# Optimization experiments

Hardware: AMD Instinct MI355X
Metric: run time of the kernel (lower is better)

## Reference

```python
import jax, jax.numpy as jnp
import numpy as np
import math

B, S, D, V = 16, 512, 64, 32000
MAX_SEQ = 512
TEMP = 1.0
EPS = 1e-12


def setup_inputs() -> dict:
    key = jax.random.key(0)
    k0, k1, k2, k3, k4 = jax.random.split(key, 5)
    tokens = jax.random.randint(k0, (B, S), 0, V)
    token_emb = jax.random.normal(k1, (V, D), dtype=jnp.float32) * 0.02
    lin_w1 = jax.random.normal(k2, (D, D), dtype=jnp.float32) * (1.0 / math.sqrt(D))
    lin_w2 = jax.random.normal(k3, (D, D), dtype=jnp.float32) * (1.0 / math.sqrt(D))
    edge_scale = jnp.full((1,), 0.1, dtype=jnp.float32)  # nn.Parameter init 0.1
    out_w = jax.random.normal(k4, (V, D), dtype=jnp.float32) * 0.02
    return {"tokens": tokens, "token_emb": token_emb, "lin_w1": lin_w1,
            "lin_w2": lin_w2, "edge_scale": edge_scale, "out_w": out_w}


def _embed(tokens, token_emb):
    # polar positional components (seq_len <= max_seq_len branch)
    pos = jnp.arange(S, dtype=jnp.float32)
    thetas = 2.0 * math.pi * (pos / MAX_SEQ)
    rs = 0.3 + 0.6 * (pos / (MAX_SEQ - 1))
    e0 = (rs * jnp.cos(thetas))[None, :, None]          # [1,S,1]
    e1 = (rs * jnp.sin(thetas))[None, :, None]          # [1,S,1]
    tok = token_emb[tokens][:, :, : D - 2]              # [B,S,D-2]
    emb = jnp.concatenate([jnp.broadcast_to(e0, (tok.shape[0], S, 1)),
                           jnp.broadcast_to(e1, (tok.shape[0], S, 1)),
                           tok], axis=-1)               # [B,S,D]
    norms = jnp.sqrt(jnp.clip(jnp.einsum('bsd,bsd->bs', emb, emb), EPS, None))
    return emb / norms[:, :, None]


def _attention(emb):
    # pairwise Euclidean distance attention, diagonal distance zeroed
    n2 = jnp.einsum('bsd,bsd->bs', emb, emb)                      # [B,S]
    dots = jnp.einsum('bqd,bkd->bqk', emb, emb)                   # [B,S,S]
    sq = n2[:, :, None] + n2[:, None, :] - 2.0 * dots
    dist = jnp.sqrt(jnp.clip(sq, EPS, None))
    dist = dist * (1.0 - jnp.eye(S, dtype=dist.dtype))[None]      # eye_mask
    return jax.nn.softmax(-dist / TEMP, axis=-1)                  # [B,S,S]


def reference(tokens, token_emb, lin_w1, lin_w2, edge_scale, out_w):
    emb = _embed(tokens, token_emb)            # [B,S,D]
    attn = _attention(emb)                     # [B,S,S]
    h = emb
    for w in (lin_w1, lin_w2):
        # message passing: x_j -> lin(x_j), edge weight = attn * edge_scale,
        # scatter-add over all incoming edges == batched attn @ h
        h = edge_scale[0] * jnp.einsum('bqk,bkd->bqd', attn, h @ w.T)
    logits = jnp.einsum('bsd,vd->bsv', h, out_w)   # [B,S,V]
    return logits
```

## Files before the change

kernel.cpp:

```cpp
#include <hip/hip_runtime.h>
#include <hip/hip_bf16.h>


#define S_ 512
#define D_ 64
#define V_ 32000

typedef __attribute__((ext_vector_type(8))) __bf16 bf16x8;
typedef __attribute__((ext_vector_type(4))) float f32x4;

__device__ inline unsigned short f2bf(float x) {
    __hip_bfloat16 h = __float2bfloat16(x);
    return __builtin_bit_cast(unsigned short, h);
}

__global__ __launch_bounds__(256) void embed_kernel(const int* __restrict__ tokens,
                                                    const float* __restrict__ temb,
                                                    float* __restrict__ emb,
                                                    float* __restrict__ n2) {
    int row  = blockIdx.x * 4 + (threadIdx.x >> 6);
    int lane = threadIdx.x & 63;
    int s    = row & (S_ - 1);
    int tok  = tokens[row];
    float val;
    if (lane < 2) {
        float fs    = (float)s;
        float theta = 6.283185307179586f * (fs * (1.0f / 512.0f));
        float r     = 0.3f + 0.6f * (fs * (1.0f / 511.0f));
        val = (lane == 0) ? r * cosf(theta) : r * sinf(theta);
    } else {
        val = temb[tok * D_ + lane - 2];
    }
    float ss = val * val;
#pragma unroll
    for (int off = 32; off; off >>= 1) ss += __shfl_xor(ss, off, 64);
    float nrm = sqrtf(fmaxf(ss, 1e-12f));
    float e   = val / nrm;
    emb[row * D_ + lane] = e;
    float nn = e * e;
#pragma unroll
    for (int off = 32; off; off >>= 1) nn += __shfl_xor(nn, off, 64);
    if (lane == 0) n2[row] = nn;
}

__global__ __launch_bounds__(128) void attn_kernel(const float* __restrict__ emb,
                                                   const float* __restrict__ n2,
                                                   const float* __restrict__ edge_scale,
                                                   float* __restrict__ attn_u,
                                                   float* __restrict__ invs) {
    __shared__ float qs[16][68];
    __shared__ float ks[64][68];
    __shared__ float n2qs[16];
    __shared__ float n2ks[64];
    int b  = blockIdx.x >> 5;
    int q0 = (blockIdx.x & 31) * 16;
    int t  = threadIdx.x;
    const float* ebase = emb + (size_t)b * S_ * D_;
#pragma unroll
    for (int j = 0; j < 2; ++j) {
        int f4 = t + j * 128;
        int r = f4 >> 4, c4 = (f4 & 15) * 4;
        *reinterpret_cast<float4*>(&qs[r][c4]) =
            *reinterpret_cast<const float4*>(&ebase[(q0 + r) * D_ + c4]);
    }
    if (t < 16) n2qs[t] = n2[b * S_ + q0 + t];

    int qg = t >> 4;
    int kg = t & 15;
    float rs[2] = {0.f, 0.f};

    for (int kt = 0; kt < 8; ++kt) {
        int k0 = kt * 64;
        __syncthreads();
#pragma unroll
        for (int j = 0; j < 8; ++j) {
            int f4 = t + j * 128;
            int r = f4 >> 4, c4 = (f4 & 15) * 4;
            *reinterpret_cast<float4*>(&ks[r][c4]) =
                *reinterpret_cast<const float4*>(&ebase[(k0 + r) * D_ + c4]);
        }
        if (t < 64) n2ks[t] = n2[b * S_ + k0 + t];
        __syncthreads();

        f32x4 acc[2][4];
#pragma unroll
        for (int i = 0; i < 2; ++i)
#pragma unroll
            for (int j = 0; j < 4; ++j) acc[i][j] = (f32x4){0.f, 0.f, 0.f, 0.f};
#pragma unroll
        for (int dc = 0; dc < 16; ++dc) {
            f32x4 qv[2], kv[4];
#pragma unroll
            for (int i = 0; i < 2; ++i) qv[i] = *reinterpret_cast<f32x4*>(&qs[qg * 2 + i][dc * 4]);
#pragma unroll
            for (int j = 0; j < 4; ++j) kv[j] = *reinterpret_cast<f32x4*>(&ks[kg * 4 + j][dc * 4]);
#pragma unroll
            for (int i = 0; i < 2; ++i)
#pragma unroll
                for (int j = 0; j < 4; ++j) acc[i][j] += qv[i] * kv[j];
        }
#pragma unroll
        for (int i = 0; i < 2; ++i) {
            int q = qg * 2 + i;
            float4 ev;
            float* evp = &ev.x;
#pragma unroll
            for (int j = 0; j < 4; ++j) {
                int k = kg * 4 + j;
                f32x4 a = acc[i][j];
                float dot = (a[0] + a[1]) + (a[2] + a[3]);
                float sq  = n2qs[q] + n2ks[k] - 2.0f * dot;
                evp[j] = (q0 + q == k0 + k) ? 1.0f : __expf(-sqrtf(fmaxf(sq, 1e-12f)));
            }
            rs[i] += (ev.x + ev.y) + (ev.z + ev.w);
            *reinterpret_cast<float4*>(
                &attn_u[((size_t)(b * S_ + q0 + q)) * S_ + k0 + kg * 4]) = ev;
        }
    }
    float scale = edge_scale[0];
#pragma unroll
    for (int i = 0; i < 2; ++i) {
#pragma unroll
        for (int off = 1; off < 16; off <<= 1) rs[i] += __shfl_xor(rs[i], off, 64);
        if (kg == 0) invs[b * S_ + q0 + qg * 2 + i] = scale / rs[i];
    }
}

__global__ __launch_bounds__(256) void proj_kernel(const float* __restrict__ h,
                                                   const float* __restrict__ w,
                                                   float* __restrict__ out) {
    __shared__ float ws[64][68];
    __shared__ float hs[16][68];
    int t  = threadIdx.x;
    int r0 = blockIdx.x * 16;
#pragma unroll
    for (int j = 0; j < 4; ++j) {
        int f4 = t + j * 256;
        int r = f4 >> 4, c4 = (f4 & 15) * 4;
        *reinterpret_cast<float4*>(&ws[r][c4]) =
            *reinterpret_cast<const float4*>(&w[r * D_ + c4]);
    }
    {
        int r = t >> 4, c4 = (t & 15) * 4;
        *reinterpret_cast<float4*>(&hs[r][c4]) =
            *reinterpret_cast<const float4*>(&h[(r0 + r) * D_ + c4]);
    }
    __syncthreads();
    int q = t >> 4, dh = t & 15;
    f32x4 acc[4];
#pragma unroll
    for (int dj = 0; dj < 4; ++dj) acc[dj] = (f32x4){0.f, 0.f, 0.f, 0.f};
#pragma unroll
    for (int ec = 0; ec < 16; ++ec) {
        f32x4 hv = *reinterpret_cast<f32x4*>(&hs[q][ec * 4]);
#pragma unroll
        for (int dj = 0; dj < 4; ++dj) {
            f32x4 wv = *reinterpret_cast<f32x4*>(&ws[dh * 4 + dj][ec * 4]);
            acc[dj] += hv * wv;
        }
    }
    float4 r;
    r.x = (acc[0][0] + acc[0][1]) + (acc[0][2] + acc[0][3]);
    r.y = (acc[1][0] + acc[1][1]) + (acc[1][2] + acc[1][3]);
    r.z = (acc[2][0] + acc[2][1]) + (acc[2][2] + acc[2][3]);
    r.w = (acc[3][0] + acc[3][1]) + (acc[3][2] + acc[3][3]);
    *reinterpret_cast<float4*>(&out[(r0 + q) * D_ + dh * 4]) = r;
}

template <bool BF16OUT>
__global__ __launch_bounds__(128) void prop_kernel(const float* __restrict__ attn_u,
                                                   const float* __restrict__ tmat,
                                                   const float* __restrict__ invs,
                                                   float* __restrict__ outf,
                                                   unsigned short* __restrict__ outb) {
    __shared__ float As[16][68];
    __shared__ float Ts[64][68];
    int b  = blockIdx.x >> 5;
    int q0 = (blockIdx.x & 31) * 16;
    int t  = threadIdx.x;
    int qg = t >> 4, dh = t & 15;
    f32x4 acc[2];
#pragma unroll
    for (int i = 0; i < 2; ++i) acc[i] = (f32x4){0.f, 0.f, 0.f, 0.f};
    const float* abase = attn_u + ((size_t)b * S_ + q0) * S_;
    const float* tbase = tmat + (size_t)b * S_ * D_;
    for (int kt = 0; kt < 8; ++kt) {
        int k0 = kt * 64;
        __syncthreads();
#pragma unroll
        for (int j = 0; j < 2; ++j) {
            int f4 = t + j * 128;
            int r = f4 >> 4, c4 = (f4 & 15) * 4;
            *reinterpret_cast<float4*>(&As[r][c4]) =
                *reinterpret_cast<const float4*>(&abase[(size_t)r * S_ + k0 + c4]);
        }
#pragma unroll
        for (int j = 0; j < 8; ++j) {
            int f4 = t + j * 128;
            int r = f4 >> 4, c4 = (f4 & 15) * 4;
            *reinterpret_cast<float4*>(&Ts[r][c4]) =
                *reinterpret_cast<const float4*>(&tbase[(k0 + r) * D_ + c4]);
        }
        __syncthreads();
#pragma unroll
        for (int kc = 0; kc < 16; ++kc) {
            f32x4 tv[4];
#pragma unroll
            for (int ks = 0; ks < 4; ++ks)
                tv[ks] = *reinterpret_cast<f32x4*>(&Ts[kc * 4 + ks][dh * 4]);
#pragma unroll
            for (int i = 0; i < 2; ++i) {
                f32x4 av = *reinterpret_cast<f32x4*>(&As[qg * 2 + i][kc * 4]);
#pragma unroll
                for (int ks = 0; ks < 4; ++ks) acc[i] += av[ks] * tv[ks];
            }
        }
    }
#pragma unroll
    for (int i = 0; i < 2; ++i) {
        int row = b * S_ + q0 + qg * 2 + i;
        float inv = invs[row];
        size_t rowbase = (size_t)row * D_ + dh * 4;
        if (BF16OUT) {
            ushort4 r;
            r.x = f2bf(inv * acc[i][0]); r.y = f2bf(inv * acc[i][1]);
            r.z = f2bf(inv * acc[i][2]); r.w = f2bf(inv * acc[i][3]);
            *reinterpret_cast<ushort4*>(&outb[rowbase]) = r;
        } else {
            *reinterpret_cast<float4*>(&outf[rowbase]) =
                make_float4(inv * acc[i][0], inv * acc[i][1],
                            inv * acc[i][2], inv * acc[i][3]);
        }
    }
}

__global__ __launch_bounds__(256) void cast_kernel(const float* __restrict__ in,
                                                   unsigned short* __restrict__ out, int n) {
    int i = (blockIdx.x * 256 + threadIdx.x) * 4;
    if (i >= n) return;
    float4 v = *reinterpret_cast<const float4*>(in + i);
    ushort4 r;
    r.x = f2bf(v.x); r.y = f2bf(v.y); r.z = f2bf(v.z); r.w = f2bf(v.w);
    *reinterpret_cast<ushort4*>(out + i) = r;
}

__global__ __launch_bounds__(256) void logits_kernel(const unsigned short* __restrict__ hb,
                                                     const unsigned short* __restrict__ wb,
                                                     float* __restrict__ out) {
    __shared__ float Ct[2][16][260];
    int bid = blockIdx.x;
    int nt = bid % 125, mt = bid / 125;
    int n0 = nt * 256, m0 = mt * 128;
    int wave = threadIdx.x >> 6, lane = threadIdx.x & 63;
    int lr = lane & 15, lh = lane >> 4;

    bf16x8 a[2][2][2];
#pragma unroll
    for (int c = 0; c < 2; ++c)
#pragma unroll
        for (int ns = 0; ns < 2; ++ns)
#pragma unroll
            for (int kh = 0; kh < 2; ++kh)
                a[c][ns][kh] = *reinterpret_cast<const bf16x8*>(
                    wb + (size_t)(n0 + wave * 64 + c * 32 + ns * 16 + lr) * D_ + kh * 32 + lh * 8);

    for (int ms = 0; ms < 8; ++ms) {
        const unsigned short* hrow = hb + (size_t)(m0 + ms * 16 + lr) * D_ + lh * 8;
        bf16x8 b0 = *reinterpret_cast<const bf16x8*>(hrow);
        bf16x8 b1 = *reinterpret_cast<const bf16x8*>(hrow + 32);
        f32x4 acc[2][2];
#pragma unroll
        for (int c = 0; c < 2; ++c)
#pragma unroll
            for (int ns = 0; ns < 2; ++ns) {
                acc[c][ns] = (f32x4){0.f, 0.f, 0.f, 0.f};
                acc[c][ns] = __builtin_amdgcn_mfma_f32_16x16x32_bf16(a[c][ns][0], b0, acc[c][ns], 0, 0, 0);
                acc[c][ns] = __builtin_amdgcn_mfma_f32_16x16x32_bf16(a[c][ns][1], b1, acc[c][ns], 0, 0, 0);
            }

        float* Lw = &Ct[ms & 1][lr][wave * 64];
#pragma unroll
        for (int c = 0; c < 2; ++c)
#pragma unroll
            for (int ns = 0; ns < 2; ++ns) {
                f32x4 v = acc[c][ns];
                *reinterpret_cast<float4*>(Lw + c * 32 + ns * 16 + lh * 4) =
                    make_float4(v[0], v[1], v[2], v[3]);
            }
        __syncthreads();

#pragma unroll
        for (int j = 0; j < 4; ++j) {
            int row = wave * 4 + j;
            const float* Lr = &Ct[ms & 1][row][lane * 4];
            float4 v = *reinterpret_cast<const float4*>(Lr);
            *reinterpret_cast<float4*>(out + (size_t)(m0 + ms * 16 + row) * V_ + n0 + lane * 4) = v;
        }
    }
}

extern "C" void kernel_launch(void* const* d_in, const int* in_sizes, int n_in,
                              void* d_out, int out_size, void* d_ws, size_t ws_size,
                              hipStream_t stream) {
    const int*   tokens = (const int*)d_in[0];
    const float* temb   = (const float*)d_in[1];
    const float* w1     = (const float*)d_in[2];
    const float* w2     = (const float*)d_in[3];
    const float* escale = (const float*)d_in[4];
    const float* outw   = (const float*)d_in[5];
    float*       out    = (float*)d_out;

    char* tail = (char*)d_out + 1048576000ull - 23068672ull;
    float* attn = (float*)(tail);
    float* emb  = (float*)(tail + 16777216);
    float* t1   = (float*)(tail + 18874368);
    float* h1   = (float*)(tail + 20971520);

    char* ws = (char*)d_ws;
    unsigned short* hb   = (unsigned short*)(ws);
    unsigned short* wb   = (unsigned short*)(ws + 1048576);
    float*          n2   = (float*)(ws + 5144576);
    float*          invs = (float*)(ws + 5177344);

    embed_kernel<<<2048, 256, 0, stream>>>(tokens, temb, emb, n2);
    attn_kernel<<<512, 128, 0, stream>>>(emb, n2, escale, attn, invs);
    cast_kernel<<<2000, 256, 0, stream>>>(outw, wb, V_ * D_);
    proj_kernel<<<512, 256, 0, stream>>>(emb, w1, t1);
    prop_kernel<false><<<512, 128, 0, stream>>>(attn, t1, invs, h1, nullptr);
    proj_kernel<<<512, 256, 0, stream>>>(h1, w2, t1);
    prop_kernel<true><<<512, 128, 0, stream>>>(attn, t1, invs, nullptr, hb);
    logits_kernel<<<8000, 256, 0, stream>>>(hb, wb, out);
}
```

Measured before the change: 290.9 us.

## Fold W2 into output weights and reassociate W1 after attention propagation

```diff
diff --git a/kernel.cpp b/kernel.cpp
--- a/kernel.cpp
+++ b/kernel.cpp
@@ -14,33 +14,77 @@
     return __builtin_bit_cast(unsigned short, h);
 }
 
-__global__ __launch_bounds__(256) void embed_kernel(const int* __restrict__ tokens,
-                                                    const float* __restrict__ temb,
-                                                    float* __restrict__ emb,
-                                                    float* __restrict__ n2) {
-    int row  = blockIdx.x * 4 + (threadIdx.x >> 6);
-    int lane = threadIdx.x & 63;
-    int s    = row & (S_ - 1);
-    int tok  = tokens[row];
-    float val;
-    if (lane < 2) {
-        float fs    = (float)s;
-        float theta = 6.283185307179586f * (fs * (1.0f / 512.0f));
-        float r     = 0.3f + 0.6f * (fs * (1.0f / 511.0f));
-        val = (lane == 0) ? r * cosf(theta) : r * sinf(theta);
+__global__ __launch_bounds__(256) void embed_wprime_kernel(const int* __restrict__ tokens,
+                                                           const float* __restrict__ temb,
+                                                           float* __restrict__ emb,
+                                                           float* __restrict__ n2,
+                                                           const float* __restrict__ outw,
+                                                           const float* __restrict__ w2,
+                                                           unsigned short* __restrict__ wb) {
+    __shared__ float os[16][68];
+    __shared__ float w2t[64][68];
+    int bid = blockIdx.x;
+    if (bid < 2048) {
+        int row  = bid * 4 + (threadIdx.x >> 6);
+        int lane = threadIdx.x & 63;
+        int s    = row & (S_ - 1);
+        int tok  = tokens[row];
+        float val;
+        if (lane < 2) {
+            float fs    = (float)s;
+            float theta = 6.283185307179586f * (fs * (1.0f / 512.0f));
+            float r     = 0.3f + 0.6f * (fs * (1.0f / 511.0f));
+            val = (lane == 0) ? r * cosf(theta) : r * sinf(theta);
+        } else {
+            val = temb[tok * D_ + lane - 2];
+        }
+        float ss = val * val;
+#pragma unroll
+        for (int off = 32; off; off >>= 1) ss += __shfl_xor(ss, off, 64);
+        float nrm = sqrtf(fmaxf(ss, 1e-12f));
+        float e   = val / nrm;
+        emb[row * D_ + lane] = e;
+        float nn = e * e;
+#pragma unroll
+        for (int off = 32; off; off >>= 1) nn += __shfl_xor(nn, off, 64);
+        if (lane == 0) n2[row] = nn;
     } else {
-        val = temb[tok * D_ + lane - 2];
-    }
-    float ss = val * val;
-#pragma unroll
-    for (int off = 32; off; off >>= 1) ss += __shfl_xor(ss, off, 64);
-    float nrm = sqrtf(fmaxf(ss, 1e-12f));
-    float e   = val / nrm;
-    emb[row * D_ + lane] = e;
-    float nn = e * e;
-#pragma unroll
-    for (int off = 32; off; off >>= 1) nn += __shfl_xor(nn, off, 64);
-    if (lane == 0) n2[row] = nn;
+        int r0 = (bid - 2048) * 16;
+        int t  = threadIdx.x;
+        {
+            int r = t >> 4, c4 = (t & 15) * 4;
+            *reinterpret_cast<float4*>(&os[r][c4]) =
+                *reinterpret_cast<const float4*>(&outw[(size_t)(r0 + r) * D_ + c4]);
+        }
+#pragma unroll
+        for (int j = 0; j < 4; ++j) {
+            int f4 = t + j * 256;
+            int d = f4 >> 4, c4 = (f4 & 15) * 4;
+            float4 v = *reinterpret_cast<const float4*>(&w2[d * D_ + c4]);
+            w2t[c4 + 0][d] = v.x; w2t[c4 + 1][d] = v.y;
+            w2t[c4 + 2][d] = v.z; w2t[c4 + 3][d] = v.w;
+        }
+        __syncthreads();
+        int q = t >> 4, eh = t & 15;
+        f32x4 acc[4];
+#pragma unroll
+        for (int ej = 0; ej < 4; ++ej) acc[ej] = (f32x4){0.f, 0.f, 0.f, 0.f};
+#pragma unroll
+        for (int dc = 0; dc < 16; ++dc) {
+            f32x4 ov = *reinterpret_cast<f32x4*>(&os[q][dc * 4]);
+#pragma unroll
+            for (int ej = 0; ej < 4; ++ej) {
+                f32x4 wv = *reinterpret_cast<f32x4*>(&w2t[eh * 4 + ej][dc * 4]);
+                acc[ej] += ov * wv;
+            }
+        }
+        ushort4 r;
+        r.x = f2bf((acc[0][0] + acc[0][1]) + (acc[0][2] + acc[0][3]));
+        r.y = f2bf((acc[1][0] + acc[1][1]) + (acc[1][2] + acc[1][3]));
+        r.z = f2bf((acc[2][0] + acc[2][1]) + (acc[2][2] + acc[2][3]));
+        r.w = f2bf((acc[3][0] + acc[3][1]) + (acc[3][2] + acc[3][3]));
+        *reinterpret_cast<ushort4*>(&wb[(size_t)(r0 + q) * D_ + eh * 4]) = r;
+    }
 }
 
 __global__ __launch_bounds__(128) void attn_kernel(const float* __restrict__ emb,
@@ -126,52 +170,104 @@
     }
 }
 
-__global__ __launch_bounds__(256) void proj_kernel(const float* __restrict__ h,
-                                                   const float* __restrict__ w,
-                                                   float* __restrict__ out) {
-    __shared__ float ws[64][68];
-    __shared__ float hs[16][68];
+__global__ __launch_bounds__(128) void prop_proj_kernel(const float* __restrict__ attn_u,
+                                                        const float* __restrict__ hsrc,
+                                                        const float* __restrict__ w1,
+                                                        const float* __restrict__ invs,
+                                                        float* __restrict__ outf) {
+    __shared__ float As[16][68];
+    __shared__ float Ts[64][68];
+    __shared__ float ws1[64][68];
+    __shared__ float gs[16][68];
+    int b  = blockIdx.x >> 5;
+    int q0 = (blockIdx.x & 31) * 16;
     int t  = threadIdx.x;
-    int r0 = blockIdx.x * 16;
-#pragma unroll
-    for (int j = 0; j < 4; ++j) {
-        int f4 = t + j * 256;
+    int qg = t >> 4, dh = t & 15;
+#pragma unroll
+    for (int j = 0; j < 8; ++j) {
+        int f4 = t + j * 128;
         int r = f4 >> 4, c4 = (f4 & 15) * 4;
-        *reinterpret_cast<float4*>(&ws[r][c4]) =
-            *reinterpret_cast<const float4*>(&w[r * D_ + c4]);
-    }
-    {
-        int r = t >> 4, c4 = (t & 15) * 4;
-        *reinterpret_cast<float4*>(&hs[r][c4]) =
-            *reinterpret_cast<const float4*>(&h[(r0 + r) * D_ + c4]);
+        *reinterpret_cast<float4*>(&ws1[r][c4]) =
+            *reinterpret_cast<const float4*>(&w1[r * D_ + c4]);
+    }
+    f32x4 acc[2];
+#pragma unroll
+    for (int i = 0; i < 2; ++i) acc[i] = (f32x4){0.f, 0.f, 0.f, 0.f};
+    const float* abase = attn_u + ((size_t)b * S_ + q0) * S_;
+    const float* tbase = hsrc + (size_t)b * S_ * D_;
+    for (int kt = 0; kt < 8; ++kt) {
+        int k0 = kt * 64;
+        __syncthreads();
+#pragma unroll
+        for (int j = 0; j < 2; ++j) {
+            int f4 = t + j * 128;
+            int r = f4 >> 4, c4 = (f4 & 15) * 4;
+            *reinterpret_cast<float4*>(&As[r][c4]) =
+                *reinterpret_cast<const float4*>(&abase[(size_t)r * S_ + k0 + c4]);
+        }
+#pragma unroll
+        for (int j = 0; j < 8; ++j) {
+            int f4 = t + j * 128;
+            int r = f4 >> 4, c4 = (f4 & 15) * 4;
+            *reinterpret_cast<float4*>(&Ts[r][c4]) =
+                *reinterpret_cast<const float4*>(&tbase[(k0 + r) * D_ + c4]);
+        }
+        __syncthreads();
+#pragma unroll
+        for (int kc = 0; kc < 16; ++kc) {
+            f32x4 tv[4];
+#pragma unroll
+            for (int ks = 0; ks < 4; ++ks)
+                tv[ks] = *reinterpret_cast<f32x4*>(&Ts[kc * 4 + ks][dh * 4]);
+#pragma unroll
+            for (int i = 0; i < 2; ++i) {
+                f32x4 av = *reinterpret_cast<f32x4*>(&As[qg * 2 + i][kc * 4]);
+#pragma unroll
+                for (int ks = 0; ks < 4; ++ks) acc[i] += av[ks] * tv[ks];
+            }
+        }
+    }
+#pragma unroll
+    for (int i = 0; i < 2; ++i) {
+        f32x4 v = acc[i];
+        *reinterpret_cast<float4*>(&gs[qg * 2 + i][dh * 4]) =
+            make_float4(v[0], v[1], v[2], v[3]);
     }
     __syncthreads();
-    int q = t >> 4, dh = t & 15;
-    f32x4 acc[4];
-#pragma unroll
-    for (int dj = 0; dj < 4; ++dj) acc[dj] = (f32x4){0.f, 0.f, 0.f, 0.f};
-#pragma unroll
-    for (int ec = 0; ec < 16; ++ec) {
-        f32x4 hv = *reinterpret_cast<f32x4*>(&hs[q][ec * 4]);
-#pragma unroll
-        for (int dj = 0; dj < 4; ++dj) {
-            f32x4 wv = *reinterpret_cast<f32x4*>(&ws[dh * 4 + dj][ec * 4]);
-            acc[dj] += hv * wv;
-        }
-    }
-    float4 r;
-    r.x = (acc[0][0] + acc[0][1]) + (acc[0][2] + acc[0][3]);
-    r.y = (acc[1][0] + acc[1][1]) + (acc[1][2] + acc[1][3]);
-    r.z = (acc[2][0] + acc[2][1]) + (acc[2][2] + acc[2][3]);
-    r.w = (acc[3][0] + acc[3][1]) + (acc[3][2] + acc[3][3]);
-    *reinterpret_cast<float4*>(&out[(r0 + q) * D_ + dh * 4]) = r;
-}
-
-template <bool BF16OUT>
+    f32x4 acc2[2][4];
+#pragma unroll
+    for (int i = 0; i < 2; ++i)
+#pragma unroll
+        for (int dj = 0; dj < 4; ++dj) acc2[i][dj] = (f32x4){0.f, 0.f, 0.f, 0.f};
+#pragma unroll
+    for (int dc = 0; dc < 16; ++dc) {
+        f32x4 wv[4];
+#pragma unroll
+        for (int dj = 0; dj < 4; ++dj)
+            wv[dj] = *reinterpret_cast<f32x4*>(&ws1[dh * 4 + dj][dc * 4]);
+#pragma unroll
+        for (int i = 0; i < 2; ++i) {
+            f32x4 gv = *reinterpret_cast<f32x4*>(&gs[qg * 2 + i][dc * 4]);
+#pragma unroll
+            for (int dj = 0; dj < 4; ++dj) acc2[i][dj] += gv * wv[dj];
+        }
+    }
+#pragma unroll
+    for (int i = 0; i < 2; ++i) {
+        int row = b * S_ + q0 + qg * 2 + i;
+        float inv = invs[row];
+        float4 r;
+        r.x = inv * ((acc2[i][0][0] + acc2[i][0][1]) + (acc2[i][0][2] + acc2[i][0][3]));
+        r.y = inv * ((acc2[i][1][0] + acc2[i][1][1]) + (acc2[i][1][2] + acc2[i][1][3]));
+        r.z = inv * ((acc2[i][2][0] + acc2[i][2][1]) + (acc2[i][2][2] + acc2[i][2][3]));
+        r.w = inv * ((acc2[i][3][0] + acc2[i][3][1]) + (acc2[i][3][2] + acc2[i][3][3]));
+        *reinterpret_cast<float4*>(&outf[(size_t)row * D_ + dh * 4]) = r;
+    }
+}
+
 __global__ __launch_bounds__(128) void prop_kernel(const float* __restrict__ attn_u,
                                                    const float* __restrict__ tmat,
                                                    const float* __restrict__ invs,
-                                                   float* __restrict__ outf,
                                                    unsigned short* __restrict__ outb) {
     __shared__ float As[16][68];
     __shared__ float Ts[64][68];
@@ -220,28 +316,11 @@
     for (int i = 0; i < 2; ++i) {
         int row = b * S_ + q0 + qg * 2 + i;
         float inv = invs[row];
-        size_t rowbase = (size_t)row * D_ + dh * 4;
-        if (BF16OUT) {
-            ushort4 r;
-            r.x = f2bf(inv * acc[i][0]); r.y = f2bf(inv * acc[i][1]);
-            r.z = f2bf(inv * acc[i][2]); r.w = f2bf(inv * acc[i][3]);
-            *reinterpret_cast<ushort4*>(&outb[rowbase]) = r;
-        } else {
-            *reinterpret_cast<float4*>(&outf[rowbase]) =
-                make_float4(inv * acc[i][0], inv * acc[i][1],
-                            inv * acc[i][2], inv * acc[i][3]);
-        }
-    }
-}
-
-__global__ __launch_bounds__(256) void cast_kernel(const float* __restrict__ in,
-                                                   unsigned short* __restrict__ out, int n) {
-    int i = (blockIdx.x * 256 + threadIdx.x) * 4;
-    if (i >= n) return;
-    float4 v = *reinterpret_cast<const float4*>(in + i);
-    ushort4 r;
-    r.x = f2bf(v.x); r.y = f2bf(v.y); r.z = f2bf(v.z); r.w = f2bf(v.w);
-    *reinterpret_cast<ushort4*>(out + i) = r;
+        ushort4 r;
+        r.x = f2bf(inv * acc[i][0]); r.y = f2bf(inv * acc[i][1]);
+        r.z = f2bf(inv * acc[i][2]); r.w = f2bf(inv * acc[i][3]);
+        *reinterpret_cast<ushort4*>(&outb[(size_t)row * D_ + dh * 4]) = r;
+    }
 }
 
 __global__ __launch_bounds__(256) void logits_kernel(const unsigned short* __restrict__ hb,
@@ -313,8 +392,7 @@
     char* tail = (char*)d_out + 1048576000ull - 23068672ull;
     float* attn = (float*)(tail);
     float* emb  = (float*)(tail + 16777216);
-    float* t1   = (float*)(tail + 18874368);
-    float* h1   = (float*)(tail + 20971520);
+    float* h1   = (float*)(tail + 18874368);
 
     char* ws = (char*)d_ws;
     unsigned short* hb   = (unsigned short*)(ws);
@@ -322,12 +400,9 @@
     float*          n2   = (float*)(ws + 5144576);
     float*          invs = (float*)(ws + 5177344);
 
-    embed_kernel<<<2048, 256, 0, stream>>>(tokens, temb, emb, n2);
+    embed_wprime_kernel<<<4048, 256, 0, stream>>>(tokens, temb, emb, n2, outw, w2, wb);
     attn_kernel<<<512, 128, 0, stream>>>(emb, n2, escale, attn, invs);
-    cast_kernel<<<2000, 256, 0, stream>>>(outw, wb, V_ * D_);
-    proj_kernel<<<512, 256, 0, stream>>>(emb, w1, t1);
-    prop_kernel<false><<<512, 128, 0, stream>>>(attn, t1, invs, h1, nullptr);
-    proj_kernel<<<512, 256, 0, stream>>>(h1, w2, t1);
-    prop_kernel<true><<<512, 128, 0, stream>>>(attn, t1, invs, nullptr, hb);
+    prop_proj_kernel<<<512, 128, 0, stream>>>(attn, emb, w1, invs, h1);
+    prop_kernel<<<512, 128, 0, stream>>>(attn, h1, invs, hb);
     logits_kernel<<<8000, 256, 0, stream>>>(hb, wb, out);
 }
```

Result: no change. 294.6 us (+1.3%).
